# Performance work log

Measured on AMD Instinct MI355X. Metric: run time of the kernel, lower is better.

Reference implementation:

```python
import jax, jax.numpy as jnp
import numpy as np

N_JOINTS = 24
JOINT_TREES = np.array([0,0,0,0,1,2,3,4,5,6,7,8,9,9,9,12,13,14,16,17,18,19,20,21])

def _build_adj():
    adj = np.eye(N_JOINTS, dtype=np.float32)
    for i, j in enumerate(JOINT_TREES):
        if i == j:
            continue
        adj[j, i] = 1.0
        adj[i, j] = 1.0
    return adj

ADJ = jnp.asarray(_build_adj())            # [N, N], with self-loops (diag=1)
MASK = jnp.ones((1, N_JOINTS, 1), jnp.float32).at[:, 0, :].set(0.0)  # root_id=0 masked

DIMS = [13, 64, 64, 64, 65]  # per_node_input -> W -> W -> W -> output_ch


def setup_inputs() -> dict:
    key = jax.random.key(0)
    ks = jax.random.split(key, 1 + 3 * 4)
    B = 65536
    inp = {"x": jax.random.normal(ks[0], (B, N_JOINTS, DIMS[0]), jnp.float32)}
    ki = 1
    for i in range(4):
        fan_in = DIMS[i]
        bound = 1.0 / np.sqrt(fan_in)
        # per-node weights (ParallelLinear, bias=False inside DensePNGCN)
        inp[f"w{i}"] = jax.random.uniform(ks[ki], (N_JOINTS, DIMS[i], DIMS[i + 1]), jnp.float32, -bound, bound); ki += 1
        # learnable adjacency weights: ~init 0.05 +- 0.05, diag forced to 1
        aw = jnp.clip(0.05 + (jax.random.uniform(ks[ki], (N_JOINTS, N_JOINTS)) - 0.5) * 0.1, 0.01, 1.0)
        aw = aw.at[jnp.arange(N_JOINTS), jnp.arange(N_JOINTS)].set(1.0)
        inp[f"aw{i}"] = aw.astype(jnp.float32); ki += 1
        # DenseWGCN bias (init zeros; random here for a non-trivial baseline)
        inp[f"b{i}"] = jax.random.normal(ks[ki], (DIMS[i + 1],), jnp.float32) * 0.01; ki += 1
    return inp


def reference(x, w0, w1, w2, w3, aw0, aw1, aw2, aw3, b0, b1, b2, b3):
    ws = [w0, w1, w2, w3]
    aws = [aw0, aw1, aw2, aw3]
    bs = [b0, b1, b2, b3]
    n = x * MASK  # mask_root: zero out root joint input
    n_layers = len(ws)
    for i in range(n_layers):
        # per-node linear (ParallelLinear, no bias)
        h = jnp.einsum('bkl,klj->bkj', n, ws[i])
        # dense weighted adjacency aggregation
        adj_w = aws[i] * ADJ  # [N, N]
        h = jnp.einsum('nm,bmj->bnj', adj_w, h)
        n = h + bs[i]
        if i + 1 < n_layers:
            n = jax.nn.relu(n)
    return n
```

## Files before the change

### kernel.cpp

```cpp
#include <hip/hip_runtime.h>


#define NJ 24
#define TB 16

typedef __attribute__((ext_vector_type(8))) short bf16x8;
typedef __attribute__((ext_vector_type(4))) float f32x4;

__device__ constexpr int NBR_OFF_C[NJ + 1] = {0,4,7,10,13,16,19,22,25,28,33,35,37,40,43,46,48,51,54,57,60,63,66,68,70};
__device__ constexpr int NBR_LIST_C[70] = {
    0,1,2,3,  0,1,4,  0,2,5,  0,3,6,  1,4,7,  2,5,8,  3,6,9,  4,7,10,
    5,8,11,  6,9,12,13,14,  7,10,  8,11,  9,12,15,  9,13,16,  9,14,17,
    12,15,  13,16,18,  14,17,19,  16,18,20,  17,19,21,  18,20,22,  19,21,23,
    20,22,  21,23
};

__device__ __forceinline__ float bf2f(unsigned short u) {
    return __uint_as_float(((unsigned int)u) << 16);
}
__device__ __forceinline__ unsigned short f2bf(float f) {
    unsigned int u = __float_as_uint(f);
    u += 0x7fffu + ((u >> 16) & 1u);
    return (unsigned short)(u >> 16);
}
__device__ __forceinline__ unsigned int pack2(float a, float b) {
    return (unsigned int)f2bf(a) | ((unsigned int)f2bf(b) << 16);
}

__global__ __launch_bounds__(256) void prepack(
    const float* __restrict__ w0, const float* __restrict__ w1,
    const float* __restrict__ w2, const float* __restrict__ w3,
    unsigned short* __restrict__ wp)
{
    const int f = blockIdx.x;
    const int t = threadIdx.x;
    const int lane = t >> 2;
    const int jp = t & 3;

    const float* w; int DIN, DOUT, joint, mt, kt;
    if (f < 96)       { w = w0; DIN = 13; DOUT = 64; int g = f;       joint = g >> 2; mt = g & 3;        kt = 0;     }
    else if (f < 288) { w = w1; DIN = 64; DOUT = 64; int g = f - 96;  joint = g >> 3; mt = (g >> 1) & 3; kt = g & 1; }
    else if (f < 480) { w = w2; DIN = 64; DOUT = 64; int g = f - 288; joint = g >> 3; mt = (g >> 1) & 3; kt = g & 1; }
    else              { w = w3; DIN = 64; DOUT = 65; int g = f - 480; joint = g / 10; int r = g % 10; mt = r >> 1; kt = r & 1; }

    const int jout = mt * 16 + (lane & 15);
    unsigned int packed = 0;
#pragma unroll
    for (int jj = 0; jj < 2; ++jj) {
        const int j = jp * 2 + jj;
        const int l = kt * 32 + (lane >> 4) * 8 + j;
        float v = 0.f;
        if (l < DIN && jout < DOUT) v = w[(joint * DIN + l) * DOUT + jout];
        packed |= (unsigned int)f2bf(v) << (16 * jj);
    }
    *(unsigned int*)(wp + (size_t)f * 512 + lane * 8 + jp * 2) = packed;
}

template<int KT, int MT>
__device__ __forceinline__ void linear_phase(unsigned short* buf, unsigned short* abuf,
    const unsigned short* __restrict__ wf, int wv, int lane)
{
    const int bl = lane & 15;
    const int quad = lane >> 4;
    const int sx = (bl & 7) << 3;
    for (int jj = 0; jj < 6; ++jj) {
        const int k = wv * 6 + jj;
        const int rbase = (k * TB + bl) * 64;
        bf16x8 bfr[KT];
#pragma unroll
        for (int kt = 0; kt < KT; ++kt)
            bfr[kt] = *(bf16x8*)&buf[rbase + ((kt * 32 + quad * 8) ^ sx)];
        const unsigned short* wj = wf + (size_t)k * (MT * KT * 512) + lane * 8;
        bf16x8 afr[MT][KT];
#pragma unroll
        for (int mt = 0; mt < MT; ++mt)
#pragma unroll
            for (int kt = 0; kt < KT; ++kt)
                afr[mt][kt] = *(const bf16x8*)(wj + (mt * KT + kt) * 512);
        f32x4 acc[MT];
#pragma unroll
        for (int mt = 0; mt < MT; ++mt) {
            acc[mt] = (f32x4){0.f, 0.f, 0.f, 0.f};
#pragma unroll
            for (int kt = 0; kt < KT; ++kt)
                acc[mt] = __builtin_amdgcn_mfma_f32_16x16x32_bf16(afr[mt][kt], bfr[kt], acc[mt], 0, 0, 0);
        }
#pragma unroll
        for (int mt = 0; mt < MT; ++mt) {
            if (mt < 4) {
                uint2 p;
                p.x = pack2(acc[mt].x, acc[mt].y);
                p.y = pack2(acc[mt].z, acc[mt].w);
                *(uint2*)&buf[rbase + ((mt * 16 + quad * 4) ^ sx)] = p;
            } else if (quad == 0) {
                abuf[k * TB + bl] = f2bf(acc[mt].x);
            }
        }
    }
}

template<bool LAST>
__device__ __forceinline__ void agg_phase(unsigned short* buf,
    const unsigned short* abuf,
    const float* __restrict__ aw, const float* __restrict__ bias,
    float* __restrict__ out, int base, int wv, int lane)
{
    const int bsub = lane >> 4;
    const int jq = lane & 15;
    const int b = wv * 4 + bsub;
    const int eo = (jq * 4) ^ ((b & 7) << 3);

    float acc[NJ][4];
#pragma unroll
    for (int n = 0; n < NJ; ++n) {
        acc[n][0] = 0.f; acc[n][1] = 0.f; acc[n][2] = 0.f; acc[n][3] = 0.f;
    }
    const float4 bv = *(const float4*)(bias + jq * 4);

#pragma unroll
    for (int m = 0; m < NJ; ++m) {
        uint2 raw = *(uint2*)&buf[(m * TB + b) * 64 + eo];
        const float h0 = __uint_as_float(raw.x << 16);
        const float h1 = __uint_as_float(raw.x & 0xffff0000u);
        const float h2 = __uint_as_float(raw.y << 16);
        const float h3 = __uint_as_float(raw.y & 0xffff0000u);
#pragma unroll
        for (int e = NBR_OFF_C[m]; e < NBR_OFF_C[m + 1]; ++e) {
            const int n = NBR_LIST_C[e];
            const float c = aw[n * NJ + m];
            acc[n][0] += c * h0; acc[n][1] += c * h1;
            acc[n][2] += c * h2; acc[n][3] += c * h3;
        }
    }

    if (!LAST) {
#pragma unroll
        for (int n = 0; n < NJ; ++n) {
            const float v0 = fmaxf(acc[n][0] + bv.x, 0.f);
            const float v1 = fmaxf(acc[n][1] + bv.y, 0.f);
            const float v2 = fmaxf(acc[n][2] + bv.z, 0.f);
            const float v3 = fmaxf(acc[n][3] + bv.w, 0.f);
            uint2 p; p.x = pack2(v0, v1); p.y = pack2(v2, v3);
            *(uint2*)&buf[(n * TB + b) * 64 + eo] = p;
        }
    } else {
        const float b64v = bias[64];
        float* ob = out + (size_t)(base + b) * (NJ * 65);
#pragma unroll
        for (int n = 0; n < NJ; ++n) {
            float* p = ob + n * 65 + jq * 4;
            p[0] = acc[n][0] + bv.x;
            p[1] = acc[n][1] + bv.y;
            p[2] = acc[n][2] + bv.z;
            p[3] = acc[n][3] + bv.w;
            if (jq == 0) {
                float s = b64v;
#pragma unroll
                for (int e = NBR_OFF_C[n]; e < NBR_OFF_C[n + 1]; ++e) {
                    const int m = NBR_LIST_C[e];
                    s += aw[n * NJ + m] * bf2f(abuf[m * TB + b]);
                }
                p[64] = s;
            }
        }
    }
}

__global__ __launch_bounds__(256, 3) void gnn_mfma(
    const float* __restrict__ x, const unsigned short* __restrict__ wp,
    const float* __restrict__ aw0, const float* __restrict__ b0,
    const float* __restrict__ aw1, const float* __restrict__ b1,
    const float* __restrict__ aw2, const float* __restrict__ b2,
    const float* __restrict__ aw3, const float* __restrict__ b3,
    float* __restrict__ out)
{
    __shared__ __align__(16) unsigned short buf[NJ * TB * 64];
    __shared__ __align__(8)  unsigned short abuf[NJ * TB];

    const int t = threadIdx.x;
    const int lane = t & 63;
    const int wv = t >> 6;
    const int base = blockIdx.x * TB;

    for (int i = t; i < NJ * TB * 16; i += 256) {
        const int k = i >> 8;
        const int b = (i >> 4) & 15;
        const int f2 = (i & 15) * 2;
        float v0 = 0.f, v1 = 0.f;
        if (k > 0) {
            const float* xr = x + (size_t)(base + b) * 312 + k * 13;
            if (f2 < 13)     v0 = xr[f2];
            if (f2 + 1 < 13) v1 = xr[f2 + 1];
        }
        const int row = k * TB + b;
        *(unsigned int*)&buf[row * 64 + (f2 ^ ((row & 7) << 3))] = pack2(v0, v1);
    }
    __syncthreads();

    linear_phase<1, 4>(buf, abuf, wp, wv, lane);
    __syncthreads();
    agg_phase<false>(buf, abuf, aw0, b0, nullptr, base, wv, lane);
    __syncthreads();
    linear_phase<2, 4>(buf, abuf, wp + 96 * 512, wv, lane);
    __syncthreads();
    agg_phase<false>(buf, abuf, aw1, b1, nullptr, base, wv, lane);
    __syncthreads();
    linear_phase<2, 4>(buf, abuf, wp + 288 * 512, wv, lane);
    __syncthreads();
    agg_phase<false>(buf, abuf, aw2, b2, nullptr, base, wv, lane);
    __syncthreads();
    linear_phase<2, 5>(buf, abuf, wp + 480 * 512, wv, lane);
    __syncthreads();
    agg_phase<true>(buf, abuf, aw3, b3, out, base, wv, lane);
}

extern "C" void kernel_launch(void* const* d_in, const int* in_sizes, int n_in,
                              void* d_out, int out_size, void* d_ws, size_t ws_size,
                              hipStream_t stream)
{
    const float* x   = (const float*)d_in[0];
    const float* w0  = (const float*)d_in[1];
    const float* aw0 = (const float*)d_in[2];
    const float* b0  = (const float*)d_in[3];
    const float* w1  = (const float*)d_in[4];
    const float* aw1 = (const float*)d_in[5];
    const float* b1  = (const float*)d_in[6];
    const float* w2  = (const float*)d_in[7];
    const float* aw2 = (const float*)d_in[8];
    const float* b2  = (const float*)d_in[9];
    const float* w3  = (const float*)d_in[10];
    const float* aw3 = (const float*)d_in[11];
    const float* b3  = (const float*)d_in[12];
    float* out = (float*)d_out;
    unsigned short* wp = (unsigned short*)d_ws;

    prepack<<<720, 256, 0, stream>>>(w0, w1, w2, w3, wp);

    const int blocks = 65536 / TB;
    gnn_mfma<<<blocks, 256, 0, stream>>>(x, wp, aw0, b0, aw1, b1,
                                         aw2, b2, aw3, b3, out);
}
```

Measured before the change: 746.0 us.

## Stage adjacency weights in LDS, cheaper bf16 rounding, parallelize channel-64 output

Copies all four 24x24 adjacency-weight matrices into shared memory once per block, so the aggregation phases read coefficients from LDS instead of global/scalar loads. The fp32-to-bf16 conversion switches from round-to-nearest-even to a simpler add-and-shift rounding, which is cheaper but differs on ties. The extra 65th output channel is now computed by 24 lanes per wave, each covering four batch rows, instead of only the lanes with jq==0 looping over every joint. Occupancy hint drops from 3 to 2 blocks per CU, which fits the larger shared-memory footprint but may reduce latency hiding.

```diff
diff --git a/kernel.cpp b/kernel.cpp
--- a/kernel.cpp
+++ b/kernel.cpp
@@ -23,8 +23,13 @@
     u += 0x7fffu + ((u >> 16) & 1u);
     return (unsigned short)(u >> 16);
 }
+__device__ __forceinline__ unsigned short f2bf_fast(float f) {
+    return (unsigned short)((__float_as_uint(f) + 0x8000u) >> 16);
+}
 __device__ __forceinline__ unsigned int pack2(float a, float b) {
-    return (unsigned int)f2bf(a) | ((unsigned int)f2bf(b) << 16);
+    const unsigned int ua = __float_as_uint(a) + 0x8000u;
+    const unsigned int ub = __float_as_uint(b) + 0x8000u;
+    return (ua >> 16) | (ub & 0xffff0000u);
 }
 
 __global__ __launch_bounds__(256) void prepack(
@@ -93,7 +98,7 @@
                 p.y = pack2(acc[mt].z, acc[mt].w);
                 *(uint2*)&buf[rbase + ((mt * 16 + quad * 4) ^ sx)] = p;
             } else if (quad == 0) {
-                abuf[k * TB + bl] = f2bf(acc[mt].x);
+                abuf[k * TB + bl] = f2bf_fast(acc[mt].x);
             }
         }
     }
@@ -101,8 +106,8 @@
 
 template<bool LAST>
 __device__ __forceinline__ void agg_phase(unsigned short* buf,
-    const unsigned short* abuf,
-    const float* __restrict__ aw, const float* __restrict__ bias,
+    const unsigned short* abuf, const float* awl,
+    const float* __restrict__ bias,
     float* __restrict__ out, int base, int wv, int lane)
 {
     const int bsub = lane >> 4;
@@ -127,7 +132,7 @@
 #pragma unroll
         for (int e = NBR_OFF_C[m]; e < NBR_OFF_C[m + 1]; ++e) {
             const int n = NBR_LIST_C[e];
-            const float c = aw[n * NJ + m];
+            const float c = awl[n * NJ + m];
             acc[n][0] += c * h0; acc[n][1] += c * h1;
             acc[n][2] += c * h2; acc[n][3] += c * h3;
         }
@@ -144,7 +149,6 @@
             *(uint2*)&buf[(n * TB + b) * 64 + eo] = p;
         }
     } else {
-        const float b64v = bias[64];
         float* ob = out + (size_t)(base + b) * (NJ * 65);
 #pragma unroll
         for (int n = 0; n < NJ; ++n) {
@@ -153,20 +157,26 @@
             p[1] = acc[n][1] + bv.y;
             p[2] = acc[n][2] + bv.z;
             p[3] = acc[n][3] + bv.w;
-            if (jq == 0) {
-                float s = b64v;
-#pragma unroll
-                for (int e = NBR_OFF_C[n]; e < NBR_OFF_C[n + 1]; ++e) {
-                    const int m = NBR_LIST_C[e];
-                    s += aw[n * NJ + m] * bf2f(abuf[m * TB + b]);
-                }
-                p[64] = s;
+        }
+        if (lane < NJ) {
+            const int n = lane;
+            const float b64v = bias[64];
+            float a64[4] = {0.f, 0.f, 0.f, 0.f};
+            for (int e = NBR_OFF_C[n]; e < NBR_OFF_C[n + 1]; ++e) {
+                const int m = NBR_LIST_C[e];
+                const float c = awl[n * NJ + m];
+#pragma unroll
+                for (int bb = 0; bb < 4; ++bb)
+                    a64[bb] += c * bf2f(abuf[m * TB + wv * 4 + bb]);
             }
-        }
-    }
-}
-
-__global__ __launch_bounds__(256, 3) void gnn_mfma(
+#pragma unroll
+            for (int bb = 0; bb < 4; ++bb)
+                out[(size_t)(base + wv * 4 + bb) * (NJ * 65) + n * 65 + 64] = a64[bb] + b64v;
+        }
+    }
+}
+
+__global__ __launch_bounds__(256, 2) void gnn_mfma(
     const float* __restrict__ x, const unsigned short* __restrict__ wp,
     const float* __restrict__ aw0, const float* __restrict__ b0,
     const float* __restrict__ aw1, const float* __restrict__ b1,
@@ -176,11 +186,19 @@
 {
     __shared__ __align__(16) unsigned short buf[NJ * TB * 64];
     __shared__ __align__(8)  unsigned short abuf[NJ * TB];
+    __shared__ __align__(16) float awl[4 * NJ * NJ];
 
     const int t = threadIdx.x;
     const int lane = t & 63;
     const int wv = t >> 6;
     const int base = blockIdx.x * TB;
+
+    for (int i = t; i < NJ * NJ; i += 256) {
+        awl[i]                = aw0[i];
+        awl[NJ * NJ + i]      = aw1[i];
+        awl[2 * NJ * NJ + i]  = aw2[i];
+        awl[3 * NJ * NJ + i]  = aw3[i];
+    }
 
     for (int i = t; i < NJ * TB * 16; i += 256) {
         const int k = i >> 8;
@@ -199,19 +217,19 @@
 
     linear_phase<1, 4>(buf, abuf, wp, wv, lane);
     __syncthreads();
-    agg_phase<false>(buf, abuf, aw0, b0, nullptr, base, wv, lane);
+    agg_phase<false>(buf, abuf, awl, b0, nullptr, base, wv, lane);
     __syncthreads();
     linear_phase<2, 4>(buf, abuf, wp + 96 * 512, wv, lane);
     __syncthreads();
-    agg_phase<false>(buf, abuf, aw1, b1, nullptr, base, wv, lane);
+    agg_phase<false>(buf, abuf, awl + NJ * NJ, b1, nullptr, base, wv, lane);
     __syncthreads();
     linear_phase<2, 4>(buf, abuf, wp + 288 * 512, wv, lane);
     __syncthreads();
-    agg_phase<false>(buf, abuf, aw2, b2, nullptr, base, wv, lane);
+    agg_phase<false>(buf, abuf, awl + 2 * NJ * NJ, b2, nullptr, base, wv, lane);
     __syncthreads();
     linear_phase<2, 5>(buf, abuf, wp + 480 * 512, wv, lane);
     __syncthreads();
-    agg_phase<true>(buf, abuf, aw3, b3, out, base, wv, lane);
+    agg_phase<true>(buf, abuf, awl + 3 * NJ * NJ, b3, out, base, wv, lane);
 }
 
 extern "C" void kernel_launch(void* const* d_in, const int* in_sizes, int n_in,
```

After: 757.8 us. About the same (+1.6%).
